# Optimization experiments

Measured on AMD Instinct MI355X. Metric: run time of the kernel, lower is better.

The kernel has to match this reference:

```python
import jax, jax.numpy as jnp
import numpy as np

N_RAYS = 16384
N_SEG = 32          # n_points - 1
N_PTS = 33
DIM = 128
N_LAYERS = 2
D_FF = 512
L_FREQ = 6
RADIUS = 3.0
SEG_LEN = 2.0 * RADIUS / N_SEG
N_HEADS = 4
D_HEAD = DIM // N_HEADS
ENC_DIM = 2 * 3 * 2 * L_FREQ   # 2 endpoints x xyz x (sin,cos) x L_FREQ = 72


def setup_inputs() -> dict:
    key = jax.random.key(0)
    ks = iter(jax.random.split(key, 40))

    def nrm(shape, fan_in):
        return jax.random.normal(next(ks), shape, dtype=jnp.float32) / np.float32(np.sqrt(fan_in))

    return {
        "points": jax.random.normal(next(ks), (N_RAYS, 6), dtype=jnp.float32),
        "W_up": nrm((ENC_DIM, DIM), ENC_DIM), "b_up": jnp.zeros((DIM,), jnp.float32),
        "ln1_s": jnp.ones((N_LAYERS, DIM), jnp.float32), "ln1_b": jnp.zeros((N_LAYERS, DIM), jnp.float32),
        "Wq": nrm((N_LAYERS, DIM, DIM), DIM), "Wk": nrm((N_LAYERS, DIM, DIM), DIM),
        "Wv": nrm((N_LAYERS, DIM, DIM), DIM), "Wo": nrm((N_LAYERS, DIM, DIM), DIM),
        "ln2_s": jnp.ones((N_LAYERS, DIM), jnp.float32), "ln2_b": jnp.zeros((N_LAYERS, DIM), jnp.float32),
        "W1": nrm((N_LAYERS, DIM, D_FF), DIM), "b1": jnp.zeros((N_LAYERS, D_FF), jnp.float32),
        "W2": nrm((N_LAYERS, D_FF, DIM), D_FF), "b2": jnp.zeros((N_LAYERS, DIM), jnp.float32),
        "w_pool": nrm((DIM,), DIM),
        "W_hit": nrm((DIM, 1), DIM), "b_hit": jnp.zeros((1,), jnp.float32),
        "W_dc": nrm((DIM, 1), DIM), "b_dc": jnp.zeros((1,), jnp.float32),
        "W_dv": nrm((DIM, 1), DIM), "b_dv": jnp.zeros((1,), jnp.float32),
    }


def _layer_norm(x, s, b):
    mu = x.mean(-1, keepdims=True)
    var = x.var(-1, keepdims=True)
    return (x - mu) * jax.lax.rsqrt(var + 1e-5) * s + b


def reference(points, W_up, b_up, ln1_s, ln1_b, Wq, Wk, Wv, Wo, ln2_s, ln2_b,
              W1, b1, W2, b2, w_pool, W_hit, b_hit, W_dc, b_dc, W_dv, b_dv):
    n = points.shape[0]
    orig = points[:, :3]
    vec = points[:, 3:] - points[:, :3]
    vec = vec / jnp.linalg.norm(vec, axis=-1, keepdims=True)

    # ray-sphere intersection (to_sphere_torch): sphere at origin, radius RADIUS
    bq = jnp.sum(orig * vec, axis=-1)
    cq = jnp.sum(orig * orig, axis=-1) - RADIUS ** 2
    sq = jnp.sqrt(jnp.maximum(bq * bq - cq, 0.0))
    t1 = -bq - sq          # (n,)
    t2 = -bq + sq

    # generate_segments: sample N_PTS along the chord, mask by t2 cutoff (ragged)
    t_values = jnp.linspace(0.0, 1.0, N_PTS, dtype=jnp.float32)[None, :] * (SEG_LEN * N_SEG) + t1[:, None]  # (n,P)
    mask = t_values[:, :-1] < t2[:, None]                                        # (n,S)
    pts = (orig[:, None, :] + vec[:, None, :] * t_values[:, :, None]) / RADIUS   # (n,P,3)
    segments = jnp.concatenate([pts[:, :-1], pts[:, 1:]], axis=-1)               # (n,S,6)

    # shrink_batch: stable compaction of valid segments to the front, zero-pad tail
    order = jnp.argsort(~mask, axis=1)                                           # stable, valid-first == descending argsort of mask
    segments = jnp.take_along_axis(segments, order[:, :, None], axis=1)
    n_left = mask.sum(axis=1)
    shrink_mask = jnp.arange(N_SEG)[None, :] < n_left[:, None]                   # get_shrink_mask
    segments = segments * shrink_mask[:, :, None]

    # encode_segments: NeRF frequency encoding of both endpoints (3-vectors)
    p2 = segments.reshape(n, N_SEG, 2, 3, 1)
    freqs = jnp.pi * (2.0 ** jnp.arange(L_FREQ, dtype=jnp.float32))
    ang = p2 * freqs                                                             # (n,S,2,3,L)
    enc = jnp.concatenate([jnp.sin(ang), jnp.cos(ang)], axis=-1).reshape(n, N_SEG, ENC_DIM)

    # net_forward: up-projection + pre-norm transformer blocks
    x = enc @ W_up + b_up                                                        # (n,S,DIM)
    scale = np.float32(1.0 / np.sqrt(D_HEAD))
    for i in range(N_LAYERS):
        h = _layer_norm(x, ln1_s[i], ln1_b[i])
        q = (h @ Wq[i]).reshape(n, N_SEG, N_HEADS, D_HEAD)
        k = (h @ Wk[i]).reshape(n, N_SEG, N_HEADS, D_HEAD)
        v = (h @ Wv[i]).reshape(n, N_SEG, N_HEADS, D_HEAD)
        att = jax.nn.softmax(jnp.einsum('nshd,nthd->nhst', q, k) * scale, axis=-1)
        o = jnp.einsum('nhst,nthd->nshd', att, v).reshape(n, N_SEG, DIM)
        x = x + o @ Wo[i]
        h = _layer_norm(x, ln2_s[i], ln2_b[i])
        x = x + jax.nn.relu(h @ W1[i] + b1[i]) @ W2[i] + b2[i]

    # heads: attention pooling -> hit logit; per-segment cls logits and dist values
    a = jax.nn.softmax(jnp.einsum('nsd,d->ns', x, w_pool), axis=-1)
    pooled = jnp.einsum('ns,nsd->nd', a, x)
    hit = (pooled @ W_hit + b_hit)[:, 0]                                         # (n,)
    dist_cls = (x @ W_dc + b_dc)[:, :, 0]                                        # (n,S)
    dist_val = jnp.clip((x @ W_dv + b_dv)[:, :, 0], 0.0, 1.0)                    # (n,S)

    # mask padded logits, argmax, un-shrink index, decode distance
    cls = jnp.where(shrink_mask, dist_cls, -jnp.inf)
    hit = jnp.where(n_left == 0, -100.0, hit)
    amax = jnp.argmax(cls, axis=1)                                               # (n,)
    gidx = jnp.take_along_axis(order, amax[:, None], axis=1)[:, 0]
    dist = (jnp.take_along_axis(dist_val, amax[:, None], axis=1)[:, 0]
            + gidx.astype(jnp.float32) * SEG_LEN + t1)
    return hit, dist
```

## Files before the change

### kernel.cpp

```cpp
#include <hip/hip_runtime.h>
#include <math.h>

#define NRAYS  16384
#define NSEG   32
#define DIM    128
#define DFF    512
#define ENCD   72
#define PXF    132
#define PH     40
#define HL     (NSEG*PH)
#define SEGL   0.1875f
#define LOOFF  405504

typedef __attribute__((ext_vector_type(8))) short short8;
typedef __attribute__((ext_vector_type(4))) float f32x4;

__device__ __forceinline__ short f2b(float x) {
    unsigned u = __float_as_uint(x);
    u += 0x7fff + ((u >> 16) & 1);
    return (short)(u >> 16);
}
__device__ __forceinline__ float b2f(short s) {
    return __uint_as_float(((unsigned)(unsigned short)s) << 16);
}
__device__ __forceinline__ void split2(float v, short &h, short &l) {
    h = f2b(v);
    l = f2b(v - b2f(h));
}

__global__ __launch_bounds__(256)
void prep_weights(const float* __restrict__ W_up, const float* __restrict__ Wq,
                  const float* __restrict__ Wk, const float* __restrict__ Wv,
                  const float* __restrict__ Wo, const float* __restrict__ W1,
                  const float* __restrict__ W2, short* __restrict__ out)
{
    int t = blockIdx.x * 256 + threadIdx.x;
    int j    = t & 7;
    int lane = (t >> 3) & 63;
    int krow = ((lane >> 4) << 3) + j;
    int ncol = lane & 15;
    float v;
    if (t < 393216) {
        int f = (t >> 9) & 7;
        int w = (t >> 12) & 3;
        int g = t >> 14;
        int kk = f >> 1, c = f & 1;
        int k = kk * 32 + krow;
        int n = w * 32 + c * 16 + ncol;
        int l = g / 12, gi = g - l * 12;
        if (gi < 4) {
            const float* s4 = (gi == 0) ? Wq : (gi == 1) ? Wk : (gi == 2) ? Wv : Wo;
            v = s4[l * 16384 + k * 128 + n];
        } else if (gi < 8) {
            v = W1[l * 65536 + k * 512 + (gi - 4) * 128 + n];
        } else {
            v = W2[l * 65536 + ((gi - 8) * 128 + k) * 128 + n];
        }
    } else {
        int t2 = t - 393216;
        int w = t2 / 3072;
        int rem = t2 - w * 3072;
        int f = rem >> 9;
        int kk = f >> 1, c = f & 1;
        int k = kk * 32 + krow;
        int n = w * 32 + c * 16 + ncol;
        v = (k < ENCD) ? W_up[k * 128 + n] : 0.0f;
    }
    short h, l2;
    split2(v, h, l2);
    out[t] = h;
    out[t + LOOFF] = l2;
}

__device__ __forceinline__ short8 lds_afrag(const short* Abuf, int rt, int kk, int lane) {
    int row  = rt * 16 + (lane & 15);
    int byte = row * 256 + kk * 64 + ((lane >> 4) << 4);
    byte ^= (row & 7) << 4;
    return *(const short8*)((const char*)Abuf + byte);
}

#define MFMA(a,b,c) __builtin_amdgcn_mfma_f32_16x16x32_bf16((a),(b),(c),0,0,0)

template<int NK>
__device__ __forceinline__ void mfma_gemm3(const short* AbH, const short* AbL,
                                           const short* BwH, f32x4 acc[2][2], int lane) {
    const short* BwL = BwH + LOOFF;
#pragma unroll
    for (int kk = 0; kk < NK; ++kk) {
        short8 ah0 = lds_afrag(AbH, 0, kk, lane);
        short8 ah1 = lds_afrag(AbH, 1, kk, lane);
        short8 al0 = lds_afrag(AbL, 0, kk, lane);
        short8 al1 = lds_afrag(AbL, 1, kk, lane);
        short8 bh0 = *(const short8*)(BwH + ((kk * 2 + 0) * 64 + lane) * 8);
        short8 bh1 = *(const short8*)(BwH + ((kk * 2 + 1) * 64 + lane) * 8);
        short8 bl0 = *(const short8*)(BwL + ((kk * 2 + 0) * 64 + lane) * 8);
        short8 bl1 = *(const short8*)(BwL + ((kk * 2 + 1) * 64 + lane) * 8);
        acc[0][0] = MFMA(ah0, bh0, acc[0][0]);
        acc[1][0] = MFMA(ah1, bh0, acc[1][0]);
        acc[0][1] = MFMA(ah0, bh1, acc[0][1]);
        acc[1][1] = MFMA(ah1, bh1, acc[1][1]);
        acc[0][0] = MFMA(al0, bh0, acc[0][0]);
        acc[1][0] = MFMA(al1, bh0, acc[1][0]);
        acc[0][1] = MFMA(al0, bh1, acc[0][1]);
        acc[1][1] = MFMA(al1, bh1, acc[1][1]);
        acc[0][0] = MFMA(ah0, bl0, acc[0][0]);
        acc[1][0] = MFMA(ah1, bl0, acc[1][0]);
        acc[0][1] = MFMA(ah0, bl1, acc[0][1]);
        acc[1][1] = MFMA(ah1, bl1, acc[1][1]);
    }
}

__device__ __forceinline__ void ln_to_Ab(const float* Xs, const float* sc, const float* bi,
                                         short* AbH, short* AbL, int t) {
    const int s = t >> 3, p = t & 7;
    const float* row = Xs + s * PXF + p * 16;
    float sum = 0.f, sq = 0.f;
#pragma unroll
    for (int j = 0; j < 16; ++j) { float v = row[j]; sum += v; sq = fmaf(v, v, sq); }
#pragma unroll
    for (int off = 1; off < 8; off <<= 1) { sum += __shfl_xor(sum, off); sq += __shfl_xor(sq, off); }
    float mu = sum * 0.0078125f;
    float rs = rsqrtf(sq * 0.0078125f - mu * mu + 1e-5f);
    short8 o0h, o1h, o0l, o1l;
#pragma unroll
    for (int j = 0; j < 8; ++j) {
        float v0 = (row[j]     - mu) * rs * sc[p * 16 + j]     + bi[p * 16 + j];
        float v1 = (row[j + 8] - mu) * rs * sc[p * 16 + 8 + j] + bi[p * 16 + 8 + j];
        short h, l;
        split2(v0, h, l); o0h[j] = h; o0l[j] = l;
        split2(v1, h, l); o1h[j] = h; o1l[j] = l;
    }
    int base = s * 256 + p * 32, swz = (s & 7) << 4;
    *(short8*)((char*)AbH + ((base)      ^ swz)) = o0h;
    *(short8*)((char*)AbH + ((base + 16) ^ swz)) = o1h;
    *(short8*)((char*)AbL + ((base)      ^ swz)) = o0l;
    *(short8*)((char*)AbL + ((base + 16) ^ swz)) = o1l;
}

__global__ __launch_bounds__(512)
void ray_tf_kernel(const float* __restrict__ points,
                   const float* __restrict__ b_up,
                   const float* __restrict__ ln1_s, const float* __restrict__ ln1_b,
                   const float* __restrict__ ln2_s, const float* __restrict__ ln2_b,
                   const float* __restrict__ b1, const float* __restrict__ b2,
                   const float* __restrict__ w_pool,
                   const float* __restrict__ W_hit, const float* __restrict__ b_hit,
                   const float* __restrict__ W_dc, const float* __restrict__ b_dc,
                   const float* __restrict__ W_dv, const float* __restrict__ b_dv,
                   const short* __restrict__ Wf,
                   float* __restrict__ out)
{
    __shared__ float Xs2[2][NSEG * PXF];
    __shared__ short AbH2[2][NSEG * DIM];
    __shared__ short AbL2[2][NSEG * DIM];
    __shared__ short Qh2[2][4 * 2 * NSEG * PH];
    __shared__ short Kh2[2][4 * 2 * NSEG * PH];
    __shared__ float LG2[2][NSEG], SCC2[2][NSEG], SCV2[2][NSEG], POOL2[2][DIM];

    const int sub  = threadIdx.x >> 8;
    const int t    = threadIdx.x & 255;
    const int lane = t & 63;
    const int w    = t >> 6;
    const int ray  = blockIdx.x * 2 + sub;

    float* X    = Xs2[sub];
    short* AbH  = AbH2[sub];
    short* AbL  = AbL2[sub];
    short* Qh   = Qh2[sub] + w * (2 * NSEG * PH);
    short* Kh   = Kh2[sub] + w * (2 * NSEG * PH);
    short* FbH  = Kh2[sub];
    short* FbL  = Kh2[sub] + 4096;
    float* LG   = LG2[sub];
    float* SCC  = SCC2[sub];
    float* SCV  = SCV2[sub];
    float* POOL = POOL2[sub];

    const float ox = points[ray*6+0], oy = points[ray*6+1], oz = points[ray*6+2];
    float dx = points[ray*6+3] - ox, dy = points[ray*6+4] - oy, dz = points[ray*6+5] - oz;
    const float dn = sqrtf(dx*dx + dy*dy + dz*dz);
    dx /= dn; dy /= dn; dz /= dn;
    const float bq = ox*dx + oy*dy + oz*dz;
    const float cq = ox*ox + oy*oy + oz*oz - 9.0f;
    const float sqv = sqrtf(fmaxf(bq*bq - cq, 0.0f));
    const float t1 = -bq - sqv, t2 = -bq + sqv;
    int n_left = 0;
#pragma unroll
    for (int j = 0; j < NSEG; ++j) {
        float tj = t1 + (float)j * SEGL;
        n_left += (tj < t2) ? 1 : 0;
    }

    for (int e = t; e < NSEG * 96; e += 256) {
        int s = e / 96, c = e - (e / 96) * 96;
        float val = 0.f;
        if (c < ENCD) {
            int ep = c / 36, rem = c - ep * 36, coord = rem / 12, u = rem - coord * 12;
            int jj = s + ep;
            float tj = t1 + (float)jj * SEGL;
            float oc = (coord == 0) ? ox : ((coord == 1) ? oy : oz);
            float vc = (coord == 0) ? dx : ((coord == 1) ? dy : dz);
            float pv = (oc + vc * tj) / 3.0f;
            if (s >= n_left) pv = 0.0f;
            int fq = (u < 6) ? u : (u - 6);
            float ang = pv * (3.14159265358979323846f * (float)(1 << fq));
            val = (u < 6) ? __sinf(ang) : __cosf(ang);
        }
        int byte = (s * 256 + c * 2) ^ ((s & 7) << 4);
        short h, l;
        split2(val, h, l);
        *(short*)((char*)AbH + byte) = h;
        *(short*)((char*)AbL + byte) = l;
    }
    __syncthreads();

    {
        f32x4 acc[2][2] = {};
        mfma_gemm3<3>(AbH, AbL, Wf + 393216 + w * 3072, acc, lane);
#pragma unroll
        for (int c = 0; c < 2; ++c) {
            int colg = w * 32 + c * 16 + (lane & 15);
            float bv = b_up[colg];
#pragma unroll
            for (int rt = 0; rt < 2; ++rt)
#pragma unroll
                for (int i = 0; i < 4; ++i) {
                    int row = rt * 16 + ((lane >> 4) << 2) + i;
                    X[row * PXF + colg] = acc[rt][c][i] + bv;
                }
        }
    }
    __syncthreads();

    const float scale = 0.17677669529663687f;

    for (int l = 0; l < 2; ++l) {
        const short* WL = Wf + l * 196608;
        ln_to_Ab(X, ln1_s + l * DIM, ln1_b + l * DIM, AbH, AbL, t);
        __syncthreads();

        f32x4 aq[2][2] = {}, ak[2][2] = {}, av[2][2] = {};
        mfma_gemm3<4>(AbH, AbL, WL + 0 * 16384 + w * 4096, aq, lane);
        mfma_gemm3<4>(AbH, AbL, WL + 1 * 16384 + w * 4096, ak, lane);
        mfma_gemm3<4>(AbH, AbL, WL + 2 * 16384 + w * 4096, av, lane);
#pragma unroll
        for (int c = 0; c < 2; ++c)
#pragma unroll
            for (int rt = 0; rt < 2; ++rt)
#pragma unroll
                for (int i = 0; i < 4; ++i) {
                    int row = rt * 16 + ((lane >> 4) << 2) + i;
                    int cl  = c * 16 + (lane & 15);
                    short h, lo;
                    split2(aq[rt][c][i], h, lo);
                    Qh[row * PH + cl] = h; Qh[HL + row * PH + cl] = lo;
                    split2(ak[rt][c][i], h, lo);
                    Kh[row * PH + cl] = h; Kh[HL + row * PH + cl] = lo;
                }
        __syncthreads();

        {
            f32x4 sA[2][2] = {};
            short8 qh[2], ql[2], kh[2], kl[2];
#pragma unroll
            for (int rt = 0; rt < 2; ++rt) {
                int byte = (rt * 16 + (lane & 15)) * (PH * 2) + ((lane >> 4) << 4);
                qh[rt] = *(const short8*)((const char*)Qh + byte);
                ql[rt] = *(const short8*)((const char*)Qh + HL * 2 + byte);
            }
#pragma unroll
            for (int ct = 0; ct < 2; ++ct) {
                int byte = (ct * 16 + (lane & 15)) * (PH * 2) + ((lane >> 4) << 4);
                kh[ct] = *(const short8*)((const char*)Kh + byte);
                kl[ct] = *(const short8*)((const char*)Kh + HL * 2 + byte);
            }
#pragma unroll
            for (int ct = 0; ct < 2; ++ct)
#pragma unroll
                for (int rt = 0; rt < 2; ++rt) {
                    sA[rt][ct] = MFMA(qh[rt], kh[ct], sA[rt][ct]);
                    sA[rt][ct] = MFMA(ql[rt], kh[ct], sA[rt][ct]);
                    sA[rt][ct] = MFMA(qh[rt], kl[ct], sA[rt][ct]);
                }

            short8 vbh[2], vbl[2];
#pragma unroll
            for (int ct = 0; ct < 2; ++ct)
#pragma unroll
                for (int j = 0; j < 8; ++j) {
                    int srcl = ((((lane >> 4) & 1) * 2 + (j >> 2)) << 4) | (lane & 15);
                    float v0 = __shfl(av[0][ct][j & 3], srcl);
                    float v1 = __shfl(av[1][ct][j & 3], srcl);
                    float vv = (lane < 32) ? v0 : v1;
                    short h, lo;
                    split2(vv, h, lo);
                    vbh[ct][j] = h; vbl[ct][j] = lo;
                }

#pragma unroll
            for (int rt = 0; rt < 2; ++rt)
#pragma unroll
                for (int i = 0; i < 4; ++i) {
                    float v0 = sA[rt][0][i] * scale, v1 = sA[rt][1][i] * scale;
                    float mx = fmaxf(v0, v1);
                    mx = fmaxf(mx, __shfl_xor(mx, 1));
                    mx = fmaxf(mx, __shfl_xor(mx, 2));
                    mx = fmaxf(mx, __shfl_xor(mx, 4));
                    mx = fmaxf(mx, __shfl_xor(mx, 8));
                    float e0 = __expf(v0 - mx), e1 = __expf(v1 - mx);
                    float sm = e0 + e1;
                    sm += __shfl_xor(sm, 1);
                    sm += __shfl_xor(sm, 2);
                    sm += __shfl_xor(sm, 4);
                    sm += __shfl_xor(sm, 8);
                    float inv = 1.0f / sm;
                    int row = rt * 16 + ((lane >> 4) << 2) + i;
                    short h, lo;
                    split2(e0 * inv, h, lo);
                    Qh[row * PH + (lane & 15)] = h;
                    Qh[HL + row * PH + (lane & 15)] = lo;
                    split2(e1 * inv, h, lo);
                    Qh[row * PH + 16 + (lane & 15)] = h;
                    Qh[HL + row * PH + 16 + (lane & 15)] = lo;
                }

            f32x4 oA[2][2] = {};
            short8 ph[2], pl[2];
#pragma unroll
            for (int rt = 0; rt < 2; ++rt) {
                int byte = (rt * 16 + (lane & 15)) * (PH * 2) + ((lane >> 4) << 4);
                ph[rt] = *(const short8*)((const char*)Qh + byte);
                pl[rt] = *(const short8*)((const char*)Qh + HL * 2 + byte);
            }
#pragma unroll
            for (int ct = 0; ct < 2; ++ct)
#pragma unroll
                for (int rt = 0; rt < 2; ++rt) {
                    oA[rt][ct] = MFMA(ph[rt], vbh[ct], oA[rt][ct]);
                    oA[rt][ct] = MFMA(pl[rt], vbh[ct], oA[rt][ct]);
                    oA[rt][ct] = MFMA(ph[rt], vbl[ct], oA[rt][ct]);
                }

#pragma unroll
            for (int rt = 0; rt < 2; ++rt)
#pragma unroll
                for (int ct = 0; ct < 2; ++ct)
#pragma unroll
                    for (int i = 0; i < 4; ++i) {
                        int row  = rt * 16 + ((lane >> 4) << 2) + i;
                        int colg = w * 32 + ct * 16 + (lane & 15);
                        int byte = (row * 256 + colg * 2) ^ ((row & 7) << 4);
                        short h, lo;
                        split2(oA[rt][ct][i], h, lo);
                        *(short*)((char*)AbH + byte) = h;
                        *(short*)((char*)AbL + byte) = lo;
                    }
        }
        __syncthreads();

        {
            f32x4 ac[2][2] = {};
            mfma_gemm3<4>(AbH, AbL, WL + 3 * 16384 + w * 4096, ac, lane);
#pragma unroll
            for (int c = 0; c < 2; ++c) {
                int colg = w * 32 + c * 16 + (lane & 15);
#pragma unroll
                for (int rt = 0; rt < 2; ++rt)
#pragma unroll
                    for (int i = 0; i < 4; ++i) {
                        int row = rt * 16 + ((lane >> 4) << 2) + i;
                        X[row * PXF + colg] += ac[rt][c][i];
                    }
            }
        }
        __syncthreads();

        ln_to_Ab(X, ln2_s + l * DIM, ln2_b + l * DIM, AbH, AbL, t);
        __syncthreads();

        for (int c4 = 0; c4 < 4; ++c4) {
            {
                f32x4 f1[2][2] = {};
                mfma_gemm3<4>(AbH, AbL, WL + (4 + c4) * 16384 + w * 4096, f1, lane);
#pragma unroll
                for (int c = 0; c < 2; ++c) {
                    int colg = w * 32 + c * 16 + (lane & 15);
                    float bv = b1[l * DFF + c4 * 128 + colg];
#pragma unroll
                    for (int rt = 0; rt < 2; ++rt)
#pragma unroll
                        for (int i = 0; i < 4; ++i) {
                            int row  = rt * 16 + ((lane >> 4) << 2) + i;
                            float v  = fmaxf(f1[rt][c][i] + bv, 0.0f);
                            int byte = (row * 256 + colg * 2) ^ ((row & 7) << 4);
                            short h, lo;
                            split2(v, h, lo);
                            *(short*)((char*)FbH + byte) = h;
                            *(short*)((char*)FbL + byte) = lo;
                        }
                }
            }
            __syncthreads();
            {
                f32x4 f2a[2][2] = {};
                mfma_gemm3<4>(FbH, FbL, WL + (8 + c4) * 16384 + w * 4096, f2a, lane);
#pragma unroll
                for (int c = 0; c < 2; ++c) {
                    int colg = w * 32 + c * 16 + (lane & 15);
                    float bv = (c4 == 0) ? b2[l * DIM + colg] : 0.0f;
#pragma unroll
                    for (int rt = 0; rt < 2; ++rt)
#pragma unroll
                        for (int i = 0; i < 4; ++i) {
                            int row = rt * 16 + ((lane >> 4) << 2) + i;
                            X[row * PXF + colg] += f2a[rt][c][i] + bv;
                        }
                }
            }
            __syncthreads();
        }
    }

    {
        const int s = t >> 3, p = t & 7;
        float acc = 0.f;
        const float* row = X + s * PXF + p * 16;
        const float* wp = w_pool + p * 16;
#pragma unroll
        for (int j = 0; j < 16; ++j) acc = fmaf(row[j], wp[j], acc);
#pragma unroll
        for (int off = 1; off < 8; off <<= 1) acc += __shfl_xor(acc, off);
        if (p == 0) LG[s] = acc;
    }
    __syncthreads();
    if (t < DIM) {
        float m = -1e30f;
        for (int s = 0; s < NSEG; ++s) m = fmaxf(m, LG[s]);
        float ssum = 0.f;
        for (int s = 0; s < NSEG; ++s) ssum += __expf(LG[s] - m);
        float inv = 1.0f / ssum;
        float acc = 0.f;
        for (int s = 0; s < NSEG; ++s) acc = fmaf(__expf(LG[s] - m), X[s * PXF + t], acc);
        POOL[t] = acc * inv;
    }
    {
        const int s = t >> 3, p = t & 7;
        float c = 0.f, v = 0.f;
        const float* row = X + s * PXF + p * 16;
#pragma unroll
        for (int j = 0; j < 16; ++j) {
            float x = row[j];
            c = fmaf(x, W_dc[p * 16 + j], c);
            v = fmaf(x, W_dv[p * 16 + j], v);
        }
#pragma unroll
        for (int off = 1; off < 8; off <<= 1) { c += __shfl_xor(c, off); v += __shfl_xor(v, off); }
        if (p == 0) {
            SCC[s] = c + b_dc[0];
            SCV[s] = fminf(fmaxf(v + b_dv[0], 0.0f), 1.0f);
        }
    }
    __syncthreads();
    if (t < 64) {
        float v = POOL[t] * W_hit[t] + POOL[t + 64] * W_hit[t + 64];
#pragma unroll
        for (int off = 1; off < 64; off <<= 1) v += __shfl_xor(v, off);
        if (t == 0) {
            float hv = v + b_hit[0];
            out[ray] = (n_left == 0) ? -100.0f : hv;
        }
    }
    if (t == 255) {
        float best = -1e30f; int am = 0;
        for (int s = 0; s < NSEG; ++s) {
            if (s < n_left) {
                float cv = SCC[s];
                if (cv > best) { best = cv; am = s; }
            }
        }
        out[NRAYS + ray] = SCV[am] + (float)am * SEGL + t1;
    }
}

extern "C" void kernel_launch(void* const* d_in, const int* in_sizes, int n_in,
                              void* d_out, int out_size, void* d_ws, size_t ws_size,
                              hipStream_t stream) {
    (void)in_sizes; (void)n_in; (void)ws_size; (void)out_size;
    const float* points = (const float*)d_in[0];
    const float* W_up   = (const float*)d_in[1];
    const float* b_up   = (const float*)d_in[2];
    const float* ln1_s  = (const float*)d_in[3];
    const float* ln1_b  = (const float*)d_in[4];
    const float* Wq     = (const float*)d_in[5];
    const float* Wk     = (const float*)d_in[6];
    const float* Wv     = (const float*)d_in[7];
    const float* Wo     = (const float*)d_in[8];
    const float* ln2_s  = (const float*)d_in[9];
    const float* ln2_b  = (const float*)d_in[10];
    const float* W1     = (const float*)d_in[11];
    const float* b1     = (const float*)d_in[12];
    const float* W2     = (const float*)d_in[13];
    const float* b2     = (const float*)d_in[14];
    const float* w_pool = (const float*)d_in[15];
    const float* W_hit  = (const float*)d_in[16];
    const float* b_hit  = (const float*)d_in[17];
    const float* W_dc   = (const float*)d_in[18];
    const float* b_dc   = (const float*)d_in[19];
    const float* W_dv   = (const float*)d_in[20];
    const float* b_dv   = (const float*)d_in[21];
    short* Wf = (short*)d_ws;
    float* out = (float*)d_out;

    hipLaunchKernelGGL(prep_weights, dim3(1584), dim3(256), 0, stream,
                       W_up, Wq, Wk, Wv, Wo, W1, W2, Wf);
    hipLaunchKernelGGL(ray_tf_kernel, dim3(NRAYS / 2), dim3(512), 0, stream,
                       points, b_up, ln1_s, ln1_b, ln2_s, ln2_b, b1, b2, w_pool,
                       W_hit, b_hit, W_dc, b_dc, W_dv, b_dv, Wf, out);
}
```

Baseline: 2.061 ms.

## Share A fragments across QKV and FFN1 GEMMs and drop a barrier

Adds a multi-output MFMA GEMM helper that loads the LN-normalized activation fragments once per k-step and reuses them across several weight matrices. It is used for the fused Q/K/V projection and for all four W1 chunks of the FFN up-projection, which removes repeated LDS fragment reads. The barrier after the Q/K scatter is removed and a barrier is placed just before the attention output overwrites the shared A buffer, relying on each wave's Q/K slice being private. Keeping sixteen FFN accumulator tiles live raises VGPR pressure and can reduce occupancy or cause spills.

```diff
diff --git a/kernel.cpp b/kernel.cpp
--- a/kernel.cpp
+++ b/kernel.cpp
@@ -110,6 +110,41 @@
     }
 }
 
+template<int NS>
+__device__ __forceinline__ void mfma_gemm3_multi(const short* AbH, const short* AbL,
+                                                 const short* B0,
+                                                 f32x4 (*accs[NS])[2], int lane) {
+#pragma unroll
+    for (int kk = 0; kk < 4; ++kk) {
+        short8 ah0 = lds_afrag(AbH, 0, kk, lane);
+        short8 ah1 = lds_afrag(AbH, 1, kk, lane);
+        short8 al0 = lds_afrag(AbL, 0, kk, lane);
+        short8 al1 = lds_afrag(AbL, 1, kk, lane);
+#pragma unroll
+        for (int s = 0; s < NS; ++s) {
+            const short* BH = B0 + s * 16384;
+            const short* BL = BH + LOOFF;
+            short8 bh0 = *(const short8*)(BH + ((kk * 2 + 0) * 64 + lane) * 8);
+            short8 bh1 = *(const short8*)(BH + ((kk * 2 + 1) * 64 + lane) * 8);
+            short8 bl0 = *(const short8*)(BL + ((kk * 2 + 0) * 64 + lane) * 8);
+            short8 bl1 = *(const short8*)(BL + ((kk * 2 + 1) * 64 + lane) * 8);
+            f32x4 (*acc)[2] = accs[s];
+            acc[0][0] = MFMA(ah0, bh0, acc[0][0]);
+            acc[1][0] = MFMA(ah1, bh0, acc[1][0]);
+            acc[0][1] = MFMA(ah0, bh1, acc[0][1]);
+            acc[1][1] = MFMA(ah1, bh1, acc[1][1]);
+            acc[0][0] = MFMA(al0, bh0, acc[0][0]);
+            acc[1][0] = MFMA(al1, bh0, acc[1][0]);
+            acc[0][1] = MFMA(al0, bh1, acc[0][1]);
+            acc[1][1] = MFMA(al1, bh1, acc[1][1]);
+            acc[0][0] = MFMA(ah0, bl0, acc[0][0]);
+            acc[1][0] = MFMA(ah1, bl0, acc[1][0]);
+            acc[0][1] = MFMA(ah0, bl1, acc[0][1]);
+            acc[1][1] = MFMA(ah1, bl1, acc[1][1]);
+        }
+    }
+}
+
 __device__ __forceinline__ void ln_to_Ab(const float* Xs, const float* sc, const float* bi,
                                          short* AbH, short* AbL, int t) {
     const int s = t >> 3, p = t & 7;
@@ -239,9 +274,10 @@
         __syncthreads();
 
         f32x4 aq[2][2] = {}, ak[2][2] = {}, av[2][2] = {};
-        mfma_gemm3<4>(AbH, AbL, WL + 0 * 16384 + w * 4096, aq, lane);
-        mfma_gemm3<4>(AbH, AbL, WL + 1 * 16384 + w * 4096, ak, lane);
-        mfma_gemm3<4>(AbH, AbL, WL + 2 * 16384 + w * 4096, av, lane);
+        {
+            f32x4 (*accs[3])[2] = { aq, ak, av };
+            mfma_gemm3_multi<3>(AbH, AbL, WL + w * 4096, accs, lane);
+        }
 #pragma unroll
         for (int c = 0; c < 2; ++c)
 #pragma unroll
@@ -256,7 +292,6 @@
                     split2(ak[rt][c][i], h, lo);
                     Kh[row * PH + cl] = h; Kh[HL + row * PH + cl] = lo;
                 }
-        __syncthreads();
 
         {
             f32x4 sA[2][2] = {};
@@ -340,6 +375,8 @@
                     oA[rt][ct] = MFMA(ph[rt], vbl[ct], oA[rt][ct]);
                 }
 
+            __syncthreads();
+
 #pragma unroll
             for (int rt = 0; rt < 2; ++rt)
 #pragma unroll
@@ -377,10 +414,13 @@
         ln_to_Ab(X, ln2_s + l * DIM, ln2_b + l * DIM, AbH, AbL, t);
         __syncthreads();
 
-        for (int c4 = 0; c4 < 4; ++c4) {
+        {
+            f32x4 f1a[4][2][2] = {};
             {
-                f32x4 f1[2][2] = {};
-                mfma_gemm3<4>(AbH, AbL, WL + (4 + c4) * 16384 + w * 4096, f1, lane);
+                f32x4 (*accs[4])[2] = { f1a[0], f1a[1], f1a[2], f1a[3] };
+                mfma_gemm3_multi<4>(AbH, AbL, WL + 4 * 16384 + w * 4096, accs, lane);
+            }
+            for (int c4 = 0; c4 < 4; ++c4) {
 #pragma unroll
                 for (int c = 0; c < 2; ++c) {
                     int colg = w * 32 + c * 16 + (lane & 15);
@@ -390,7 +430,7 @@
 #pragma unroll
                         for (int i = 0; i < 4; ++i) {
                             int row  = rt * 16 + ((lane >> 4) << 2) + i;
-                            float v  = fmaxf(f1[rt][c][i] + bv, 0.0f);
+                            float v  = fmaxf(f1a[c4][rt][c][i] + bv, 0.0f);
                             int byte = (row * 256 + colg * 2) ^ ((row & 7) << 4);
                             short h, lo;
                             split2(v, h, lo);
@@ -398,25 +438,25 @@
                             *(short*)((char*)FbL + byte) = lo;
                         }
                 }
-            }
-            __syncthreads();
-            {
-                f32x4 f2a[2][2] = {};
-                mfma_gemm3<4>(FbH, FbL, WL + (8 + c4) * 16384 + w * 4096, f2a, lane);
-#pragma unroll
-                for (int c = 0; c < 2; ++c) {
-                    int colg = w * 32 + c * 16 + (lane & 15);
-                    float bv = (c4 == 0) ? b2[l * DIM + colg] : 0.0f;
-#pragma unroll
-                    for (int rt = 0; rt < 2; ++rt)
-#pragma unroll
-                        for (int i = 0; i < 4; ++i) {
-                            int row = rt * 16 + ((lane >> 4) << 2) + i;
-                            X[row * PXF + colg] += f2a[rt][c][i] + bv;
-                        }
-                }
-            }
-            __syncthreads();
+                __syncthreads();
+                {
+                    f32x4 f2a[2][2] = {};
+                    mfma_gemm3<4>(FbH, FbL, WL + (8 + c4) * 16384 + w * 4096, f2a, lane);
+#pragma unroll
+                    for (int c = 0; c < 2; ++c) {
+                        int colg = w * 32 + c * 16 + (lane & 15);
+                        float bv = (c4 == 0) ? b2[l * DIM + colg] : 0.0f;
+#pragma unroll
+                        for (int rt = 0; rt < 2; ++rt)
+#pragma unroll
+                            for (int i = 0; i < 4; ++i) {
+                                int row = rt * 16 + ((lane >> 4) << 2) + i;
+                                X[row * PXF + colg] += f2a[rt][c][i] + bv;
+                            }
+                    }
+                }
+                __syncthreads();
+            }
         }
     }
 
```

Measured after the change: 3.057 ms. 48.3% more time.

## Share A fragments across QKV and FFN1 GEMMs, move barrier after attention

Applied to the files above, without the earlier changes.

Merges the Q/K/V projections into one k-loop that loads each LDS A fragment once and streams three weight sets. It does the same for all four FFN1 chunks, computing them up front into four accumulator sets before the FFN2 passes. The barrier after the Q/K stores is moved to after the P·V MFMAs, before the AbH/AbL overwrite. This cuts LDS A-fragment reads but raises register pressure (up to 16 f32x4 accumulators held live), which may lower occupancy or cause spills. Dropping the barrier before the QK^T reads looks risky unless each wave only reads the Q/K columns it wrote itself.

```diff
diff --git a/kernel.cpp b/kernel.cpp
--- a/kernel.cpp
+++ b/kernel.cpp
@@ -81,32 +81,37 @@
 
 #define MFMA(a,b,c) __builtin_amdgcn_mfma_f32_16x16x32_bf16((a),(b),(c),0,0,0)
 
+#define STREAM12(BH_, acc) do { \
+    const short* BH_m = (BH_); \
+    const short* BL_m = BH_m + LOOFF; \
+    short8 bh0 = *(const short8*)(BH_m + ((kk * 2 + 0) * 64 + lane) * 8); \
+    short8 bh1 = *(const short8*)(BH_m + ((kk * 2 + 1) * 64 + lane) * 8); \
+    short8 bl0 = *(const short8*)(BL_m + ((kk * 2 + 0) * 64 + lane) * 8); \
+    short8 bl1 = *(const short8*)(BL_m + ((kk * 2 + 1) * 64 + lane) * 8); \
+    acc[0][0] = MFMA(ah0, bh0, acc[0][0]); \
+    acc[1][0] = MFMA(ah1, bh0, acc[1][0]); \
+    acc[0][1] = MFMA(ah0, bh1, acc[0][1]); \
+    acc[1][1] = MFMA(ah1, bh1, acc[1][1]); \
+    acc[0][0] = MFMA(al0, bh0, acc[0][0]); \
+    acc[1][0] = MFMA(al1, bh0, acc[1][0]); \
+    acc[0][1] = MFMA(al0, bh1, acc[0][1]); \
+    acc[1][1] = MFMA(al1, bh1, acc[1][1]); \
+    acc[0][0] = MFMA(ah0, bl0, acc[0][0]); \
+    acc[1][0] = MFMA(ah1, bl0, acc[1][0]); \
+    acc[0][1] = MFMA(ah0, bl1, acc[0][1]); \
+    acc[1][1] = MFMA(ah1, bl1, acc[1][1]); \
+} while (0)
+
 template<int NK>
 __device__ __forceinline__ void mfma_gemm3(const short* AbH, const short* AbL,
                                            const short* BwH, f32x4 acc[2][2], int lane) {
-    const short* BwL = BwH + LOOFF;
 #pragma unroll
     for (int kk = 0; kk < NK; ++kk) {
         short8 ah0 = lds_afrag(AbH, 0, kk, lane);
         short8 ah1 = lds_afrag(AbH, 1, kk, lane);
         short8 al0 = lds_afrag(AbL, 0, kk, lane);
         short8 al1 = lds_afrag(AbL, 1, kk, lane);
-        short8 bh0 = *(const short8*)(BwH + ((kk * 2 + 0) * 64 + lane) * 8);
-        short8 bh1 = *(const short8*)(BwH + ((kk * 2 + 1) * 64 + lane) * 8);
-        short8 bl0 = *(const short8*)(BwL + ((kk * 2 + 0) * 64 + lane) * 8);
-        short8 bl1 = *(const short8*)(BwL + ((kk * 2 + 1) * 64 + lane) * 8);
-        acc[0][0] = MFMA(ah0, bh0, acc[0][0]);
-        acc[1][0] = MFMA(ah1, bh0, acc[1][0]);
-        acc[0][1] = MFMA(ah0, bh1, acc[0][1]);
-        acc[1][1] = MFMA(ah1, bh1, acc[1][1]);
-        acc[0][0] = MFMA(al0, bh0, acc[0][0]);
-        acc[1][0] = MFMA(al1, bh0, acc[1][0]);
-        acc[0][1] = MFMA(al0, bh1, acc[0][1]);
-        acc[1][1] = MFMA(al1, bh1, acc[1][1]);
-        acc[0][0] = MFMA(ah0, bl0, acc[0][0]);
-        acc[1][0] = MFMA(ah1, bl0, acc[1][0]);
-        acc[0][1] = MFMA(ah0, bl1, acc[0][1]);
-        acc[1][1] = MFMA(ah1, bl1, acc[1][1]);
+        STREAM12(BwH, acc);
     }
 }
 
@@ -239,9 +244,16 @@
         __syncthreads();
 
         f32x4 aq[2][2] = {}, ak[2][2] = {}, av[2][2] = {};
-        mfma_gemm3<4>(AbH, AbL, WL + 0 * 16384 + w * 4096, aq, lane);
-        mfma_gemm3<4>(AbH, AbL, WL + 1 * 16384 + w * 4096, ak, lane);
-        mfma_gemm3<4>(AbH, AbL, WL + 2 * 16384 + w * 4096, av, lane);
+#pragma unroll
+        for (int kk = 0; kk < 4; ++kk) {
+            short8 ah0 = lds_afrag(AbH, 0, kk, lane);
+            short8 ah1 = lds_afrag(AbH, 1, kk, lane);
+            short8 al0 = lds_afrag(AbL, 0, kk, lane);
+            short8 al1 = lds_afrag(AbL, 1, kk, lane);
+            STREAM12(WL + 0 * 16384 + w * 4096, aq);
+            STREAM12(WL + 1 * 16384 + w * 4096, ak);
+            STREAM12(WL + 2 * 16384 + w * 4096, av);
+        }
 #pragma unroll
         for (int c = 0; c < 2; ++c)
 #pragma unroll
@@ -256,7 +268,6 @@
                     split2(ak[rt][c][i], h, lo);
                     Kh[row * PH + cl] = h; Kh[HL + row * PH + cl] = lo;
                 }
-        __syncthreads();
 
         {
             f32x4 sA[2][2] = {};
@@ -340,6 +351,8 @@
                     oA[rt][ct] = MFMA(ph[rt], vbl[ct], oA[rt][ct]);
                 }
 
+            __syncthreads();
+
 #pragma unroll
             for (int rt = 0; rt < 2; ++rt)
 #pragma unroll
@@ -377,46 +390,63 @@
         ln_to_Ab(X, ln2_s + l * DIM, ln2_b + l * DIM, AbH, AbL, t);
         __syncthreads();
 
-        for (int c4 = 0; c4 < 4; ++c4) {
-            {
-                f32x4 f1[2][2] = {};
-                mfma_gemm3<4>(AbH, AbL, WL + (4 + c4) * 16384 + w * 4096, f1, lane);
-#pragma unroll
-                for (int c = 0; c < 2; ++c) {
-                    int colg = w * 32 + c * 16 + (lane & 15);
-                    float bv = b1[l * DFF + c4 * 128 + colg];
-#pragma unroll
-                    for (int rt = 0; rt < 2; ++rt)
-#pragma unroll
-                        for (int i = 0; i < 4; ++i) {
-                            int row  = rt * 16 + ((lane >> 4) << 2) + i;
-                            float v  = fmaxf(f1[rt][c][i] + bv, 0.0f);
-                            int byte = (row * 256 + colg * 2) ^ ((row & 7) << 4);
-                            short h, lo;
-                            split2(v, h, lo);
-                            *(short*)((char*)FbH + byte) = h;
-                            *(short*)((char*)FbL + byte) = lo;
-                        }
-                }
+        {
+            f32x4 f0[2][2] = {}, f1[2][2] = {}, f2c[2][2] = {}, f3[2][2] = {};
+#pragma unroll
+            for (int kk = 0; kk < 4; ++kk) {
+                short8 ah0 = lds_afrag(AbH, 0, kk, lane);
+                short8 ah1 = lds_afrag(AbH, 1, kk, lane);
+                short8 al0 = lds_afrag(AbL, 0, kk, lane);
+                short8 al1 = lds_afrag(AbL, 1, kk, lane);
+                STREAM12(WL + 4 * 16384 + w * 4096, f0);
+                STREAM12(WL + 5 * 16384 + w * 4096, f1);
+                STREAM12(WL + 6 * 16384 + w * 4096, f2c);
+                STREAM12(WL + 7 * 16384 + w * 4096, f3);
             }
-            __syncthreads();
-            {
-                f32x4 f2a[2][2] = {};
-                mfma_gemm3<4>(FbH, FbL, WL + (8 + c4) * 16384 + w * 4096, f2a, lane);
-#pragma unroll
-                for (int c = 0; c < 2; ++c) {
-                    int colg = w * 32 + c * 16 + (lane & 15);
-                    float bv = (c4 == 0) ? b2[l * DIM + colg] : 0.0f;
-#pragma unroll
-                    for (int rt = 0; rt < 2; ++rt)
-#pragma unroll
-                        for (int i = 0; i < 4; ++i) {
-                            int row = rt * 16 + ((lane >> 4) << 2) + i;
-                            X[row * PXF + colg] += f2a[rt][c][i] + bv;
-                        }
-                }
-            }
-            __syncthreads();
+
+#define FFN_CHUNK(c4, facc) do { \
+    _Pragma("unroll") \
+    for (int c = 0; c < 2; ++c) { \
+        int colg = w * 32 + c * 16 + (lane & 15); \
+        float bv = b1[l * DFF + (c4) * 128 + colg]; \
+        _Pragma("unroll") \
+        for (int rt = 0; rt < 2; ++rt) \
+            _Pragma("unroll") \
+            for (int i = 0; i < 4; ++i) { \
+                int row  = rt * 16 + ((lane >> 4) << 2) + i; \
+                float v  = fmaxf(facc[rt][c][i] + bv, 0.0f); \
+                int byte = (row * 256 + colg * 2) ^ ((row & 7) << 4); \
+                short h, lo; \
+                split2(v, h, lo); \
+                *(short*)((char*)FbH + byte) = h; \
+                *(short*)((char*)FbL + byte) = lo; \
+            } \
+    } \
+    __syncthreads(); \
+    { \
+        f32x4 f2a[2][2] = {}; \
+        mfma_gemm3<4>(FbH, FbL, WL + (8 + (c4)) * 16384 + w * 4096, f2a, lane); \
+        _Pragma("unroll") \
+        for (int c = 0; c < 2; ++c) { \
+            int colg = w * 32 + c * 16 + (lane & 15); \
+            float bv = ((c4) == 0) ? b2[l * DIM + colg] : 0.0f; \
+            _Pragma("unroll") \
+            for (int rt = 0; rt < 2; ++rt) \
+                _Pragma("unroll") \
+                for (int i = 0; i < 4; ++i) { \
+                    int row = rt * 16 + ((lane >> 4) << 2) + i; \
+                    X[row * PXF + colg] += f2a[rt][c][i] + bv; \
+                } \
+        } \
+    } \
+    __syncthreads(); \
+} while (0)
+
+            FFN_CHUNK(0, f0);
+            FFN_CHUNK(1, f1);
+            FFN_CHUNK(2, f2c);
+            FFN_CHUNK(3, f3);
+#undef FFN_CHUNK
         }
     }
 
```

Result: slower. 2.649 ms (+28.5%).

## Drop attention barrier and double-buffer FFN hidden chunks to cut syncs

Applied to the files above, without the earlier changes.

The Q and K projections are now written to per-wave LDS slices and consumed by the same wave, so the block-wide barrier between the QKV GEMMs and the score MFMAs is removed. A single barrier is placed instead just before the attention output overwrites the shared AbH/AbL buffers. The FFN loop is unrolled with two ping-ponged hidden buffers (reusing the Kh and Qh regions), which removes one barrier per chunk. Accumulator scopes are also tightened to reduce register pressure. The risks are a fragile reliance on wave-local LDS ordering and a longer unrolled code body.

```diff
diff --git a/kernel.cpp b/kernel.cpp
--- a/kernel.cpp
+++ b/kernel.cpp
@@ -168,8 +168,10 @@
     short* AbL  = AbL2[sub];
     short* Qh   = Qh2[sub] + w * (2 * NSEG * PH);
     short* Kh   = Kh2[sub] + w * (2 * NSEG * PH);
-    short* FbH  = Kh2[sub];
-    short* FbL  = Kh2[sub] + 4096;
+    short* Fb0H = Kh2[sub];
+    short* Fb0L = Kh2[sub] + 4096;
+    short* Fb1H = Qh2[sub];
+    short* Fb1L = Qh2[sub] + 4096;
     float* LG   = LG2[sub];
     float* SCC  = SCC2[sub];
     float* SCV  = SCV2[sub];
@@ -238,51 +240,42 @@
         ln_to_Ab(X, ln1_s + l * DIM, ln1_b + l * DIM, AbH, AbL, t);
         __syncthreads();
 
-        f32x4 aq[2][2] = {}, ak[2][2] = {}, av[2][2] = {};
-        mfma_gemm3<4>(AbH, AbL, WL + 0 * 16384 + w * 4096, aq, lane);
-        mfma_gemm3<4>(AbH, AbL, WL + 1 * 16384 + w * 4096, ak, lane);
-        mfma_gemm3<4>(AbH, AbL, WL + 2 * 16384 + w * 4096, av, lane);
-#pragma unroll
-        for (int c = 0; c < 2; ++c)
-#pragma unroll
-            for (int rt = 0; rt < 2; ++rt)
-#pragma unroll
-                for (int i = 0; i < 4; ++i) {
-                    int row = rt * 16 + ((lane >> 4) << 2) + i;
-                    int cl  = c * 16 + (lane & 15);
-                    short h, lo;
-                    split2(aq[rt][c][i], h, lo);
-                    Qh[row * PH + cl] = h; Qh[HL + row * PH + cl] = lo;
-                    split2(ak[rt][c][i], h, lo);
-                    Kh[row * PH + cl] = h; Kh[HL + row * PH + cl] = lo;
-                }
-        __syncthreads();
-
         {
-            f32x4 sA[2][2] = {};
-            short8 qh[2], ql[2], kh[2], kl[2];
-#pragma unroll
-            for (int rt = 0; rt < 2; ++rt) {
-                int byte = (rt * 16 + (lane & 15)) * (PH * 2) + ((lane >> 4) << 4);
-                qh[rt] = *(const short8*)((const char*)Qh + byte);
-                ql[rt] = *(const short8*)((const char*)Qh + HL * 2 + byte);
-            }
-#pragma unroll
-            for (int ct = 0; ct < 2; ++ct) {
-                int byte = (ct * 16 + (lane & 15)) * (PH * 2) + ((lane >> 4) << 4);
-                kh[ct] = *(const short8*)((const char*)Kh + byte);
-                kl[ct] = *(const short8*)((const char*)Kh + HL * 2 + byte);
-            }
-#pragma unroll
-            for (int ct = 0; ct < 2; ++ct)
-#pragma unroll
-                for (int rt = 0; rt < 2; ++rt) {
-                    sA[rt][ct] = MFMA(qh[rt], kh[ct], sA[rt][ct]);
-                    sA[rt][ct] = MFMA(ql[rt], kh[ct], sA[rt][ct]);
-                    sA[rt][ct] = MFMA(qh[rt], kl[ct], sA[rt][ct]);
-                }
-
-            short8 vbh[2], vbl[2];
+            f32x4 aq[2][2] = {};
+            mfma_gemm3<4>(AbH, AbL, WL + 0 * 16384 + w * 4096, aq, lane);
+#pragma unroll
+            for (int c = 0; c < 2; ++c)
+#pragma unroll
+                for (int rt = 0; rt < 2; ++rt)
+#pragma unroll
+                    for (int i = 0; i < 4; ++i) {
+                        int row = rt * 16 + ((lane >> 4) << 2) + i;
+                        int cl  = c * 16 + (lane & 15);
+                        short h, lo;
+                        split2(aq[rt][c][i], h, lo);
+                        Qh[row * PH + cl] = h; Qh[HL + row * PH + cl] = lo;
+                    }
+        }
+        {
+            f32x4 ak[2][2] = {};
+            mfma_gemm3<4>(AbH, AbL, WL + 1 * 16384 + w * 4096, ak, lane);
+#pragma unroll
+            for (int c = 0; c < 2; ++c)
+#pragma unroll
+                for (int rt = 0; rt < 2; ++rt)
+#pragma unroll
+                    for (int i = 0; i < 4; ++i) {
+                        int row = rt * 16 + ((lane >> 4) << 2) + i;
+                        int cl  = c * 16 + (lane & 15);
+                        short h, lo;
+                        split2(ak[rt][c][i], h, lo);
+                        Kh[row * PH + cl] = h; Kh[HL + row * PH + cl] = lo;
+                    }
+        }
+        short8 vbh[2], vbl[2];
+        {
+            f32x4 av[2][2] = {};
+            mfma_gemm3<4>(AbH, AbL, WL + 2 * 16384 + w * 4096, av, lane);
 #pragma unroll
             for (int ct = 0; ct < 2; ++ct)
 #pragma unroll
@@ -295,6 +288,33 @@
                     split2(vv, h, lo);
                     vbh[ct][j] = h; vbl[ct][j] = lo;
                 }
+        }
+
+        {
+            f32x4 sA[2][2] = {};
+            {
+                short8 qh[2], ql[2], kh[2], kl[2];
+#pragma unroll
+                for (int rt = 0; rt < 2; ++rt) {
+                    int byte = (rt * 16 + (lane & 15)) * (PH * 2) + ((lane >> 4) << 4);
+                    qh[rt] = *(const short8*)((const char*)Qh + byte);
+                    ql[rt] = *(const short8*)((const char*)Qh + HL * 2 + byte);
+                }
+#pragma unroll
+                for (int ct = 0; ct < 2; ++ct) {
+                    int byte = (ct * 16 + (lane & 15)) * (PH * 2) + ((lane >> 4) << 4);
+                    kh[ct] = *(const short8*)((const char*)Kh + byte);
+                    kl[ct] = *(const short8*)((const char*)Kh + HL * 2 + byte);
+                }
+#pragma unroll
+                for (int ct = 0; ct < 2; ++ct)
+#pragma unroll
+                    for (int rt = 0; rt < 2; ++rt) {
+                        sA[rt][ct] = MFMA(qh[rt], kh[ct], sA[rt][ct]);
+                        sA[rt][ct] = MFMA(ql[rt], kh[ct], sA[rt][ct]);
+                        sA[rt][ct] = MFMA(qh[rt], kl[ct], sA[rt][ct]);
+                    }
+            }
 
 #pragma unroll
             for (int rt = 0; rt < 2; ++rt)
@@ -324,21 +344,25 @@
                 }
 
             f32x4 oA[2][2] = {};
-            short8 ph[2], pl[2];
-#pragma unroll
-            for (int rt = 0; rt < 2; ++rt) {
-                int byte = (rt * 16 + (lane & 15)) * (PH * 2) + ((lane >> 4) << 4);
-                ph[rt] = *(const short8*)((const char*)Qh + byte);
-                pl[rt] = *(const short8*)((const char*)Qh + HL * 2 + byte);
+            {
+                short8 ph[2], pl[2];
+#pragma unroll
+                for (int rt = 0; rt < 2; ++rt) {
+                    int byte = (rt * 16 + (lane & 15)) * (PH * 2) + ((lane >> 4) << 4);
+                    ph[rt] = *(const short8*)((const char*)Qh + byte);
+                    pl[rt] = *(const short8*)((const char*)Qh + HL * 2 + byte);
+                }
+#pragma unroll
+                for (int ct = 0; ct < 2; ++ct)
+#pragma unroll
+                    for (int rt = 0; rt < 2; ++rt) {
+                        oA[rt][ct] = MFMA(ph[rt], vbh[ct], oA[rt][ct]);
+                        oA[rt][ct] = MFMA(pl[rt], vbh[ct], oA[rt][ct]);
+                        oA[rt][ct] = MFMA(ph[rt], vbl[ct], oA[rt][ct]);
+                    }
             }
-#pragma unroll
-            for (int ct = 0; ct < 2; ++ct)
-#pragma unroll
-                for (int rt = 0; rt < 2; ++rt) {
-                    oA[rt][ct] = MFMA(ph[rt], vbh[ct], oA[rt][ct]);
-                    oA[rt][ct] = MFMA(pl[rt], vbh[ct], oA[rt][ct]);
-                    oA[rt][ct] = MFMA(ph[rt], vbl[ct], oA[rt][ct]);
-                }
+
+            __syncthreads();
 
 #pragma unroll
             for (int rt = 0; rt < 2; ++rt)
@@ -377,47 +401,60 @@
         ln_to_Ab(X, ln2_s + l * DIM, ln2_b + l * DIM, AbH, AbL, t);
         __syncthreads();
 
-        for (int c4 = 0; c4 < 4; ++c4) {
-            {
-                f32x4 f1[2][2] = {};
-                mfma_gemm3<4>(AbH, AbL, WL + (4 + c4) * 16384 + w * 4096, f1, lane);
-#pragma unroll
-                for (int c = 0; c < 2; ++c) {
-                    int colg = w * 32 + c * 16 + (lane & 15);
-                    float bv = b1[l * DFF + c4 * 128 + colg];
-#pragma unroll
-                    for (int rt = 0; rt < 2; ++rt)
-#pragma unroll
-                        for (int i = 0; i < 4; ++i) {
-                            int row  = rt * 16 + ((lane >> 4) << 2) + i;
-                            float v  = fmaxf(f1[rt][c][i] + bv, 0.0f);
-                            int byte = (row * 256 + colg * 2) ^ ((row & 7) << 4);
-                            short h, lo;
-                            split2(v, h, lo);
-                            *(short*)((char*)FbH + byte) = h;
-                            *(short*)((char*)FbL + byte) = lo;
-                        }
-                }
-            }
-            __syncthreads();
-            {
-                f32x4 f2a[2][2] = {};
-                mfma_gemm3<4>(FbH, FbL, WL + (8 + c4) * 16384 + w * 4096, f2a, lane);
-#pragma unroll
-                for (int c = 0; c < 2; ++c) {
-                    int colg = w * 32 + c * 16 + (lane & 15);
-                    float bv = (c4 == 0) ? b2[l * DIM + colg] : 0.0f;
-#pragma unroll
-                    for (int rt = 0; rt < 2; ++rt)
-#pragma unroll
-                        for (int i = 0; i < 4; ++i) {
-                            int row = rt * 16 + ((lane >> 4) << 2) + i;
-                            X[row * PXF + colg] += f2a[rt][c][i] + bv;
-                        }
-                }
-            }
-            __syncthreads();
-        }
+#define FFN_W1(c4, FH, FL) do { \
+    f32x4 f1[2][2] = {}; \
+    mfma_gemm3<4>(AbH, AbL, WL + (4 + (c4)) * 16384 + w * 4096, f1, lane); \
+    _Pragma("unroll") \
+    for (int c = 0; c < 2; ++c) { \
+        int colg = w * 32 + c * 16 + (lane & 15); \
+        float bv = b1[l * DFF + (c4) * 128 + colg]; \
+        _Pragma("unroll") \
+        for (int rt = 0; rt < 2; ++rt) \
+            _Pragma("unroll") \
+            for (int i = 0; i < 4; ++i) { \
+                int row  = rt * 16 + ((lane >> 4) << 2) + i; \
+                float v  = fmaxf(f1[rt][c][i] + bv, 0.0f); \
+                int byte = (row * 256 + colg * 2) ^ ((row & 7) << 4); \
+                short h, lo; \
+                split2(v, h, lo); \
+                *(short*)((char*)(FH) + byte) = h; \
+                *(short*)((char*)(FL) + byte) = lo; \
+            } \
+    } \
+} while (0)
+
+#define FFN_W2(c4, FH, FL) do { \
+    f32x4 f2a[2][2] = {}; \
+    mfma_gemm3<4>((FH), (FL), WL + (8 + (c4)) * 16384 + w * 4096, f2a, lane); \
+    _Pragma("unroll") \
+    for (int c = 0; c < 2; ++c) { \
+        int colg = w * 32 + c * 16 + (lane & 15); \
+        float bv = ((c4) == 0) ? b2[l * DIM + colg] : 0.0f; \
+        _Pragma("unroll") \
+        for (int rt = 0; rt < 2; ++rt) \
+            _Pragma("unroll") \
+            for (int i = 0; i < 4; ++i) { \
+                int row = rt * 16 + ((lane >> 4) << 2) + i; \
+                X[row * PXF + colg] += f2a[rt][c][i] + bv; \
+            } \
+    } \
+} while (0)
+
+        FFN_W1(0, Fb0H, Fb0L);
+        __syncthreads();
+        FFN_W2(0, Fb0H, Fb0L);
+        FFN_W1(1, Fb1H, Fb1L);
+        __syncthreads();
+        FFN_W2(1, Fb1H, Fb1L);
+        FFN_W1(2, Fb0H, Fb0L);
+        __syncthreads();
+        FFN_W2(2, Fb0H, Fb0L);
+        FFN_W1(3, Fb1H, Fb1L);
+        __syncthreads();
+        FFN_W2(3, Fb1H, Fb1L);
+        __syncthreads();
+#undef FFN_W1
+#undef FFN_W2
     }
 
     {
```

Measured after the change: 1.893 ms (median of 2 runs). -8.1%, faster.
